# Kernel optimization log

Hardware: AMD Instinct MI355X
Metric: run time of the kernel (lower is better)

Reference implementation:

```python
import jax, jax.numpy as jnp
import numpy as np

T, N, E = 8, 10000, 200000
F_IN, H, OUT = 32, 128, 64
EPS = 1e-5


def setup_inputs() -> dict:
    key = jax.random.key(0)
    ks = jax.random.split(key, 28)
    inp = {}
    inp['x'] = jax.random.normal(ks[0], (T, N, F_IN), jnp.float32)
    inp['edge_index'] = jax.random.randint(ks[1], (2, E), 0, N, dtype=jnp.int32)
    # GCN layer weights (Glorot-ish scale)
    inp['w_gcn0'] = jax.random.normal(ks[2], (F_IN, H), jnp.float32) / np.float32(np.sqrt(F_IN))
    inp['b_gcn0'] = jnp.zeros((H,), jnp.float32)
    inp['w_gcn1'] = jax.random.normal(ks[3], (H, H), jnp.float32) / np.float32(np.sqrt(H))
    inp['b_gcn1'] = jnp.zeros((H,), jnp.float32)
    inp['w_gcn2'] = jax.random.normal(ks[4], (H, H), jnp.float32) / np.float32(np.sqrt(H))
    inp['b_gcn2'] = jnp.zeros((H,), jnp.float32)
    # BatchNorm (eval mode) params for the two inner norms
    for i, kb in zip(range(2), range(5, 9, 2)):
        inp[f'bn_g{i}'] = 1.0 + 0.1 * jax.random.normal(ks[kb], (H,), jnp.float32)
        inp[f'bn_b{i}'] = 0.1 * jax.random.normal(ks[kb + 1], (H,), jnp.float32)
        inp[f'bn_m{i}'] = 0.1 * jax.random.normal(ks[kb + 10], (H,), jnp.float32)
        inp[f'bn_v{i}'] = jax.random.uniform(ks[kb + 11], (H,), jnp.float32, 0.5, 1.5)
    # 3-layer LSTM params, torch gate order (i, f, g, o)
    s = np.float32(1.0 / np.sqrt(OUT))
    dims_in = [H, OUT, OUT]
    for l in range(3):
        k0, k1, k2, k3 = jax.random.split(ks[20 + l], 4)
        inp[f'w_ih_{l}'] = jax.random.uniform(k0, (4 * OUT, dims_in[l]), jnp.float32, -s, s)
        inp[f'w_hh_{l}'] = jax.random.uniform(k1, (4 * OUT, OUT), jnp.float32, -s, s)
        inp[f'b_ih_{l}'] = jax.random.uniform(k2, (4 * OUT,), jnp.float32, -s, s)
        inp[f'b_hh_{l}'] = jax.random.uniform(k3, (4 * OUT,), jnp.float32, -s, s)
    return inp


def reference(x, edge_index, w_gcn0, b_gcn0, w_gcn1, b_gcn1, w_gcn2, b_gcn2,
              bn_g0, bn_b0, bn_m0, bn_v0, bn_g1, bn_b1, bn_m1, bn_v1,
              w_ih_0, w_hh_0, b_ih_0, b_hh_0,
              w_ih_1, w_hh_1, b_ih_1, b_hh_1,
              w_ih_2, w_hh_2, b_ih_2, b_hh_2):
    src, dst = edge_index[0], edge_index[1]
    # symmetric GCN normalization with self-loops: deg = in-degree + 1
    deg = jax.ops.segment_sum(jnp.ones((E,), x.dtype), dst, num_segments=N) + 1.0
    dis = jax.lax.rsqrt(deg)
    coef = dis[src] * dis[dst]          # [E] edge norm
    self_w = dis * dis                   # [N] self-loop norm

    def gcn(h, W, b):
        hw = jnp.einsum('tnf,fo->tno', h, W)                      # [T,N,O]
        msg = hw[:, src, :] * coef[None, :, None]                  # [T,E,O]
        agg = jax.vmap(lambda m: jax.ops.segment_sum(m, dst, num_segments=N))(msg)
        return agg + hw * self_w[None, :, None] + b

    def bn(h, g, b_, m, v):  # eval-mode BatchNorm1d
        return (h - m) * (g * jax.lax.rsqrt(v + EPS)) + b_

    h = bn(jax.nn.relu(gcn(x, w_gcn0, b_gcn0)), bn_g0, bn_b0, bn_m0, bn_v0)
    h = bn(jax.nn.relu(gcn(h, w_gcn1, b_gcn1)), bn_g1, bn_b1, bn_m1, bn_v1)
    h = jax.nn.relu(gcn(h, w_gcn2, b_gcn2))                        # [T,N,H]

    def lstm_layer(xs, Wih, Whh, bih, bhh):
        Hd = Whh.shape[1]
        bias = bih + bhh
        def step(carry, xt):
            hp, cp = carry
            g = xt @ Wih.T + hp @ Whh.T + bias
            i, f, gg, o = jnp.split(g, 4, axis=-1)
            c = jax.nn.sigmoid(f) * cp + jax.nn.sigmoid(i) * jnp.tanh(gg)
            hn = jax.nn.sigmoid(o) * jnp.tanh(c)
            return (hn, c), hn
        z = jnp.zeros((xs.shape[1], Hd), xs.dtype)
        _, ys = jax.lax.scan(step, (z, z), xs)
        return ys  # [T,N,Hd]

    ys = lstm_layer(h, w_ih_0, w_hh_0, b_ih_0, b_hh_0)
    ys = lstm_layer(ys, w_ih_1, w_hh_1, b_ih_1, b_hh_1)
    ys = lstm_layer(ys, w_ih_2, w_hh_2, b_ih_2, b_hh_2)
    return ys[-1]  # [N, OUT] == x[:, -1, :] in the torch code
```

## Files before the change

### kernel.cpp

```cpp
#include <hip/hip_runtime.h>
#include <hip/hip_bf16.h>
#include <math.h>

#define NTHREADS 256
#define T_STEPS 8
#define F_INC 32
#define H_DIM 128
#define O_DIM 64

typedef unsigned short u16;
typedef __attribute__((ext_vector_type(8))) short short8_t;
typedef __attribute__((ext_vector_type(4))) float float4_t;

__device__ __forceinline__ float bf2f(u16 u) {
    return __uint_as_float(((unsigned)u) << 16);
}
__device__ __forceinline__ u16 f2bf(float f) {
    __hip_bfloat16 h = __float2bfloat16(f);
    union { __hip_bfloat16 h; u16 s; } cv; cv.h = h; return cv.s;
}
__device__ __forceinline__ void bf8_unpack(uint4 u, float* f) {
    f[0] = __uint_as_float(u.x << 16); f[1] = __uint_as_float(u.x & 0xffff0000u);
    f[2] = __uint_as_float(u.y << 16); f[3] = __uint_as_float(u.y & 0xffff0000u);
    f[4] = __uint_as_float(u.z << 16); f[5] = __uint_as_float(u.z & 0xffff0000u);
    f[6] = __uint_as_float(u.w << 16); f[7] = __uint_as_float(u.w & 0xffff0000u);
}
__device__ __forceinline__ float fsig(float x) {
    float xc = fminf(fmaxf(x, -30.f), 30.f);
    float e = __builtin_amdgcn_exp2f(xc * -1.4426950408889634f);
    return __builtin_amdgcn_rcpf(1.0f + e);
}
__device__ __forceinline__ float ftanh(float x) {
    float xc = fminf(fmaxf(x, -15.f), 15.f);
    float e = __builtin_amdgcn_exp2f(xc * -2.8853900817779268f);
    float r = __builtin_amdgcn_rcpf(1.0f + e);
    return fmaf(-2.0f * e, r, 1.0f);
}

__global__ void count_kernel(const int* __restrict__ ei, int* __restrict__ cnt, int E) {
    int e = blockIdx.x * NTHREADS + threadIdx.x;
    if (e < E) atomicAdd(&cnt[ei[E + e]], 1);
}

__global__ void scan_part1(const int* __restrict__ cnt, int* __restrict__ bsum, int n) {
    __shared__ int sd[NTHREADS];
    const int i = blockIdx.x * NTHREADS + threadIdx.x;
    sd[threadIdx.x] = (i < n) ? cnt[i] : 0;
    __syncthreads();
    for (int off = 128; off > 0; off >>= 1) {
        if (threadIdx.x < off) sd[threadIdx.x] += sd[threadIdx.x + off];
        __syncthreads();
    }
    if (threadIdx.x == 0) bsum[blockIdx.x] = sd[0];
}

__global__ void scan_part3(const int* __restrict__ cnt, const int* __restrict__ bsum,
                           int* __restrict__ rowptr, int* __restrict__ wp,
                           float* __restrict__ dis, float* __restrict__ selfw, int n) {
    __shared__ int sd[NTHREADS];
    __shared__ int sbase;
    const int tid = threadIdx.x;
    if (tid < 64) {
        int v0 = (tid < blockIdx.x) ? bsum[tid] : 0;
        #pragma unroll
        for (int off = 1; off < 64; off <<= 1) v0 += __shfl_xor(v0, off);
        if (tid == 0) sbase = v0;
    }
    const int i = blockIdx.x * NTHREADS + tid;
    const int v = (i < n) ? cnt[i] : 0;
    sd[tid] = v;
    __syncthreads();
    for (int off = 1; off < NTHREADS; off <<= 1) {
        const int tv = (tid >= off) ? sd[tid - off] : 0;
        __syncthreads();
        sd[tid] += tv;
        __syncthreads();
    }
    const int excl = sbase + sd[tid] - v;
    if (i < n) {
        rowptr[i] = excl; wp[i] = excl;
        if (i == n - 1) rowptr[n] = excl + v;
        const float d = 1.0f + (float)v;
        dis[i] = rsqrtf(d);
        selfw[i] = 1.0f / d;
    }
}

__global__ void fill_kernel(const int* __restrict__ ei, const float* __restrict__ dis,
                            int* __restrict__ wp, int* __restrict__ csr_src,
                            float* __restrict__ coefA, int E) {
    int e = blockIdx.x * NTHREADS + threadIdx.x;
    if (e < E) {
        int s = ei[e], d = ei[E + e];
        int p = atomicAdd(&wp[d], 1);
        csr_src[p] = s;
        coefA[p] = dis[s] * dis[d];
    }
}

__global__ void wprep_all_kernel(const float* g0, const float* g1, const float* g2,
                                 const float* i0, const float* i1, const float* i2,
                                 const float* h0, const float* h1, const float* h2,
                                 u16* o_g0, u16* o_g1, u16* o_g2,
                                 u16* o_i0, u16* o_i1, u16* o_i2,
                                 u16* o_h0, u16* o_h1, u16* o_h2) {
    const int i = blockIdx.x * NTHREADS + threadIdx.x;
    if (i < 4096)        { o_g0[i] = f2bf(g0[(i & 31) * 128 + (i >> 5)]); }
    else if (i < 20480)  { int j = i - 4096;   o_g1[j] = f2bf(g1[(j & 127) * 128 + (j >> 7)]); }
    else if (i < 36864)  { int j = i - 20480;  o_g2[j] = f2bf(g2[(j & 127) * 128 + (j >> 7)]); }
    else if (i < 69632)  { int j = i - 36864;  o_i0[j] = f2bf(i0[j]); }
    else if (i < 86016)  { int j = i - 69632;  o_i1[j] = f2bf(i1[j]); }
    else if (i < 102400) { int j = i - 86016;  o_i2[j] = f2bf(i2[j]); }
    else if (i < 118784) { int j = i - 102400; o_h0[j] = f2bf(h0[j]); }
    else if (i < 135168) { int j = i - 118784; o_h1[j] = f2bf(h1[j]); }
    else if (i < 151552) { int j = i - 135168; o_h2[j] = f2bf(h2[j]); }
}

__global__ __launch_bounds__(NTHREADS)
void gcn32_kernel(const float* __restrict__ x, const int* __restrict__ rowptr,
                  const int* __restrict__ csrc, const float* __restrict__ coefA,
                  const float* __restrict__ selfw, const u16* __restrict__ Wt,
                  const float* __restrict__ bias,
                  const float* __restrict__ bng, const float* __restrict__ bnb,
                  const float* __restrict__ bnm, const float* __restrict__ bnv,
                  u16* __restrict__ out, int N) {
    constexpr int ASTR = 40;
    __shared__ __align__(16) u16 aT[16][ASTR];
    const int t = blockIdx.x;
    const int n0 = blockIdx.y * 16;
    const int tid = threadIdx.x;
    const int wid = tid >> 6, lane = tid & 63;
    const int quad = lane >> 4, l16 = lane & 15;
    const float* xb = x + (long)t * N * 32;

    const int split = lane >> 3;
    const int c4 = (lane & 7) * 4;
    for (int i = 0; i < 4; ++i) {
        const int n = n0 + wid * 4 + i;
        const int e0 = rowptr[n], e1 = rowptr[n + 1];
        float a[4] = {};
        #pragma unroll 2
        for (int e = e0 + split; e < e1; e += 8) {
            const float wgt = coefA[e];
            const int s = csrc[e];
            const float4 v = *(const float4*)(xb + (long)s * 32 + c4);
            a[0] = fmaf(wgt, v.x, a[0]);
            a[1] = fmaf(wgt, v.y, a[1]);
            a[2] = fmaf(wgt, v.z, a[2]);
            a[3] = fmaf(wgt, v.w, a[3]);
        }
        #pragma unroll
        for (int j = 0; j < 4; ++j) {
            a[j] += __shfl_xor(a[j], 8);
            a[j] += __shfl_xor(a[j], 16);
            a[j] += __shfl_xor(a[j], 32);
        }
        if (split == 0) {
            const float sw = selfw[n];
            const float4 sv = *(const float4*)(xb + (long)n * 32 + c4);
            ushort4 o;
            o.x = f2bf(fmaf(sw, sv.x, a[0]));
            o.y = f2bf(fmaf(sw, sv.y, a[1]));
            o.z = f2bf(fmaf(sw, sv.z, a[2]));
            o.w = f2bf(fmaf(sw, sv.w, a[3]));
            *(ushort4*)(&aT[wid * 4 + i][c4]) = o;
        }
    }
    __syncthreads();

    const short8_t fA = *(const short8_t*)(&aT[l16][quad * 8]);
    float4_t acc[2];
    short8_t fB[2];
    #pragma unroll
    for (int ct = 0; ct < 2; ++ct) {
        const int col = wid * 32 + ct * 16 + l16;
        fB[ct] = *(const short8_t*)(Wt + (long)col * 32 + quad * 8);
        acc[ct] = (float4_t){0.f, 0.f, 0.f, 0.f};
    }
    #pragma unroll
    for (int ct = 0; ct < 2; ++ct)
        acc[ct] = __builtin_amdgcn_mfma_f32_16x16x32_bf16(fA, fB[ct], acc[ct], 0, 0, 0);

    #pragma unroll
    for (int ct = 0; ct < 2; ++ct) {
        const int c = wid * 32 + ct * 16 + l16;
        const float s = bng[c] * rsqrtf(bnv[c] + 1e-5f);
        const float a1 = bnb[c] - bnm[c] * s;
        const float a0 = bias[c];
        #pragma unroll
        for (int r = 0; r < 4; ++r) {
            const int node = quad * 4 + r;
            float v = fmaf(fmaxf(acc[ct][r] + a0, 0.f), s, a1);
            out[((long)t * N + n0 + node) * 128 + c] = f2bf(v);
        }
    }
}

template<int EPI>
__global__ __launch_bounds__(NTHREADS)
void gcn128_kernel(const u16* __restrict__ h, const int* __restrict__ rowptr,
                   const int* __restrict__ csrc, const float* __restrict__ coefA,
                   const float* __restrict__ selfw, const u16* __restrict__ Wt,
                   const float* __restrict__ bias,
                   const float* __restrict__ bng, const float* __restrict__ bnb,
                   const float* __restrict__ bnm, const float* __restrict__ bnv,
                   u16* __restrict__ out, int N) {
    constexpr int ASTR = 136;
    __shared__ __align__(16) u16 aT[16][ASTR];
    const int t = blockIdx.x;
    const int n0 = blockIdx.y * 16;
    const int tid = threadIdx.x;
    const int wid = tid >> 6, lane = tid & 63;
    const int quad = lane >> 4, l16 = lane & 15;
    const u16* hb = h + (long)t * N * 128;

    const int split = lane >> 4;
    const int c8 = l16 * 8;
    for (int i = 0; i < 4; ++i) {
        const int n = n0 + wid * 4 + i;
        const int e0 = rowptr[n], e1 = rowptr[n + 1];
        float a[8] = {};
        #pragma unroll 2
        for (int e = e0 + split; e < e1; e += 4) {
            const float wgt = coefA[e];
            const int s = csrc[e];
            const uint4 v = *(const uint4*)(hb + (long)s * 128 + c8);
            float f[8];
            bf8_unpack(v, f);
            #pragma unroll
            for (int j = 0; j < 8; ++j) a[j] = fmaf(wgt, f[j], a[j]);
        }
        #pragma unroll
        for (int j = 0; j < 8; ++j) {
            a[j] += __shfl_xor(a[j], 16);
            a[j] += __shfl_xor(a[j], 32);
        }
        if (split == 0) {
            const float sw = selfw[n];
            const uint4 sv = *(const uint4*)(hb + (long)n * 128 + c8);
            float f[8];
            bf8_unpack(sv, f);
            ushort4 o0, o1;
            o0.x = f2bf(fmaf(sw, f[0], a[0])); o0.y = f2bf(fmaf(sw, f[1], a[1]));
            o0.z = f2bf(fmaf(sw, f[2], a[2])); o0.w = f2bf(fmaf(sw, f[3], a[3]));
            o1.x = f2bf(fmaf(sw, f[4], a[4])); o1.y = f2bf(fmaf(sw, f[5], a[5]));
            o1.z = f2bf(fmaf(sw, f[6], a[6])); o1.w = f2bf(fmaf(sw, f[7], a[7]));
            *(ushort4*)(&aT[wid * 4 + i][c8]) = o0;
            *(ushort4*)(&aT[wid * 4 + i][c8 + 4]) = o1;
        }
    }
    __syncthreads();

    short8_t fA[4];
    #pragma unroll
    for (int ks = 0; ks < 4; ++ks)
        fA[ks] = *(const short8_t*)(&aT[l16][ks * 32 + quad * 8]);
    float4_t acc[2];
    #pragma unroll
    for (int ct = 0; ct < 2; ++ct) acc[ct] = (float4_t){0.f, 0.f, 0.f, 0.f};
    #pragma unroll
    for (int ct = 0; ct < 2; ++ct) {
        const int col = wid * 32 + ct * 16 + l16;
        #pragma unroll
        for (int ks = 0; ks < 4; ++ks) {
            const short8_t fB = *(const short8_t*)(Wt + (long)col * 128 + ks * 32 + quad * 8);
            acc[ct] = __builtin_amdgcn_mfma_f32_16x16x32_bf16(fA[ks], fB, acc[ct], 0, 0, 0);
        }
    }

    #pragma unroll
    for (int ct = 0; ct < 2; ++ct) {
        const int c = wid * 32 + ct * 16 + l16;
        const float a0 = bias[c];
        float s = 0.f, a1 = 0.f;
        if constexpr (EPI == 2) {
            s = bng[c] * rsqrtf(bnv[c] + 1e-5f);
            a1 = bnb[c] - bnm[c] * s;
        }
        #pragma unroll
        for (int r = 0; r < 4; ++r) {
            const int node = quad * 4 + r;
            float v = fmaxf(acc[ct][r] + a0, 0.f);
            if constexpr (EPI == 2) v = fmaf(v, s, a1);
            out[((long)t * N + n0 + node) * 128 + c] = f2bf(v);
        }
    }
}

template<int KIN, bool IN_SPLIT, bool LAST>
__global__ __launch_bounds__(NTHREADS, 2)
void lstm_layer_kernel(const u16* __restrict__ in_hi, const u16* __restrict__ in_lo,
                       const u16* __restrict__ wih, const u16* __restrict__ whh,
                       const float* __restrict__ bi, const float* __restrict__ bh,
                       u16* __restrict__ out_hi, u16* __restrict__ out_lo,
                       float* __restrict__ out_f, int N) {
    constexpr int NKS = KIN / 32;
    constexpr int HSTR = 76;
    const int tid = threadIdx.x;
    const int w = tid >> 6, lane = tid & 63;
    const int quad = lane >> 4, l16 = lane & 15;
    const int n0 = blockIdx.x * 16;
    const int u = w * 16 + l16;

    __shared__ __align__(16) u16 hT[2][16][HSTR];
    for (int p = tid; p < 2 * 16 * HSTR; p += NTHREADS) (&hT[0][0][0])[p] = 0;

    short8_t fI[4][NKS], fH[4][2];
    #pragma unroll
    for (int g = 0; g < 4; ++g) {
        #pragma unroll
        for (int ks = 0; ks < NKS; ++ks)
            fI[g][ks] = *(const short8_t*)(wih + (long)(g * 64 + u) * KIN + ks * 32 + quad * 8);
        #pragma unroll
        for (int ks = 0; ks < 2; ++ks)
            fH[g][ks] = *(const short8_t*)(whh + (long)(g * 64 + u) * 64 + ks * 32 + quad * 8);
    }
    float bias[4];
    #pragma unroll
    for (int g = 0; g < 4; ++g) bias[g] = bi[g * 64 + u] + bh[g * 64 + u];
    float cst[4] = {};
    __syncthreads();

    #pragma unroll 1
    for (int t = 0; t < T_STEPS; ++t) {
        short8_t ain[NKS], ainl[NKS];
        const long ibase = ((long)t * N + n0 + l16) * KIN + quad * 8;
        #pragma unroll
        for (int ks = 0; ks < NKS; ++ks) {
            ain[ks] = *(const short8_t*)(in_hi + ibase + ks * 32);
            if constexpr (IN_SPLIT) ainl[ks] = *(const short8_t*)(in_lo + ibase + ks * 32);
        }
        short8_t ah[2], al[2];
        #pragma unroll
        for (int ks = 0; ks < 2; ++ks) {
            ah[ks] = *(const short8_t*)(&hT[0][l16][ks * 32 + quad * 8]);
            al[ks] = *(const short8_t*)(&hT[1][l16][ks * 32 + quad * 8]);
        }
        __syncthreads();

        float4_t acc[4];
        #pragma unroll
        for (int g = 0; g < 4; ++g) acc[g] = (float4_t){bias[g], bias[g], bias[g], bias[g]};
        #pragma unroll
        for (int ks = 0; ks < NKS; ++ks)
            #pragma unroll
            for (int g = 0; g < 4; ++g) {
                acc[g] = __builtin_amdgcn_mfma_f32_16x16x32_bf16(ain[ks], fI[g][ks], acc[g], 0, 0, 0);
                if constexpr (IN_SPLIT)
                    acc[g] = __builtin_amdgcn_mfma_f32_16x16x32_bf16(ainl[ks], fI[g][ks], acc[g], 0, 0, 0);
            }
        #pragma unroll
        for (int ks = 0; ks < 2; ++ks)
            #pragma unroll
            for (int g = 0; g < 4; ++g) {
                acc[g] = __builtin_amdgcn_mfma_f32_16x16x32_bf16(ah[ks], fH[g][ks], acc[g], 0, 0, 0);
                acc[g] = __builtin_amdgcn_mfma_f32_16x16x32_bf16(al[ks], fH[g][ks], acc[g], 0, 0, 0);
            }

        #pragma unroll
        for (int r = 0; r < 4; ++r) {
            const float si = fsig(acc[0][r]);
            const float sf = fsig(acc[1][r]);
            const float gg = ftanh(acc[2][r]);
            const float so = fsig(acc[3][r]);
            const float c = sf * cst[r] + si * gg;
            cst[r] = c;
            const float h = so * ftanh(c);
            const int node = quad * 4 + r;
            const u16 hi = f2bf(h);
            const u16 lo = f2bf(h - bf2f(hi));
            hT[0][node][u] = hi;
            hT[1][node][u] = lo;
            if constexpr (LAST) {
                if (t == T_STEPS - 1) out_f[(long)(n0 + node) * 64 + u] = h;
            } else {
                const long o = ((long)t * N + n0 + node) * 64 + u;
                out_hi[o] = hi;
                out_lo[o] = lo;
            }
        }
        __syncthreads();
    }
}

extern "C" void kernel_launch(void* const* d_in, const int* in_sizes, int n_in,
                              void* d_out, int out_size, void* d_ws, size_t ws_size,
                              hipStream_t stream) {
    (void)n_in; (void)out_size; (void)ws_size;
    const float* x      = (const float*)d_in[0];
    const int*   ei     = (const int*)d_in[1];
    const float* w_gcn0 = (const float*)d_in[2];
    const float* b_gcn0 = (const float*)d_in[3];
    const float* w_gcn1 = (const float*)d_in[4];
    const float* b_gcn1 = (const float*)d_in[5];
    const float* w_gcn2 = (const float*)d_in[6];
    const float* b_gcn2 = (const float*)d_in[7];
    const float* bn_g0  = (const float*)d_in[8];
    const float* bn_b0  = (const float*)d_in[9];
    const float* bn_m0  = (const float*)d_in[10];
    const float* bn_v0  = (const float*)d_in[11];
    const float* bn_g1  = (const float*)d_in[12];
    const float* bn_b1  = (const float*)d_in[13];
    const float* bn_m1  = (const float*)d_in[14];
    const float* bn_v1  = (const float*)d_in[15];
    const float* w_ih_0 = (const float*)d_in[16];
    const float* w_hh_0 = (const float*)d_in[17];
    const float* b_ih_0 = (const float*)d_in[18];
    const float* b_hh_0 = (const float*)d_in[19];
    const float* w_ih_1 = (const float*)d_in[20];
    const float* w_hh_1 = (const float*)d_in[21];
    const float* b_ih_1 = (const float*)d_in[22];
    const float* b_hh_1 = (const float*)d_in[23];
    const float* w_ih_2 = (const float*)d_in[24];
    const float* w_hh_2 = (const float*)d_in[25];
    const float* b_ih_2 = (const float*)d_in[26];
    const float* b_hh_2 = (const float*)d_in[27];

    const int E = in_sizes[1] / 2;
    const int N = in_sizes[0] / (T_STEPS * F_INC);
    const long M = (long)N * T_STEPS;

    char* ws = (char*)d_ws;
    size_t off = 0;
    auto carve = [&](size_t bytes) -> void* {
        void* p = ws + off;
        off += (bytes + 255) & ~(size_t)255;
        return p;
    };
    float* dis     = (float*)carve((size_t)N * 4);
    float* selfw   = (float*)carve((size_t)N * 4);
    float* coefA   = (float*)carve((size_t)E * 4);
    int*   cnt     = (int*)carve((size_t)N * 4);
    int*   rowptr  = (int*)carve((size_t)(N + 1) * 4);
    int*   wp      = (int*)carve((size_t)N * 4);
    int*   csr_src = (int*)carve((size_t)E * 4);
    int*   bsum    = (int*)carve(64 * 4);
    u16*   hbuf    = (u16*)carve((size_t)M * H_DIM * 2);
    u16*   hbuf2   = (u16*)carve((size_t)M * H_DIM * 2);
    u16*   pA_hi   = (u16*)carve((size_t)M * O_DIM * 2);
    u16*   pA_lo   = (u16*)carve((size_t)M * O_DIM * 2);
    u16*   pB_hi   = (u16*)carve((size_t)M * O_DIM * 2);
    u16*   pB_lo   = (u16*)carve((size_t)M * O_DIM * 2);
    u16*   wt0     = (u16*)carve((size_t)128 * 32 * 2);
    u16*   wt1     = (u16*)carve((size_t)128 * 128 * 2);
    u16*   wt2     = (u16*)carve((size_t)128 * 128 * 2);
    u16*   wtih0   = (u16*)carve((size_t)256 * 128 * 2);
    u16*   wtih1   = (u16*)carve((size_t)256 * 64 * 2);
    u16*   wtih2   = (u16*)carve((size_t)256 * 64 * 2);
    u16*   whh0b   = (u16*)carve((size_t)256 * 64 * 2);
    u16*   whh1b   = (u16*)carve((size_t)256 * 64 * 2);
    u16*   whh2b   = (u16*)carve((size_t)256 * 64 * 2);

    const dim3 b256(NTHREADS);
    const int gN = (N + NTHREADS - 1) / NTHREADS;
    const int gE = (E + NTHREADS - 1) / NTHREADS;

    hipMemsetAsync(cnt, 0, (size_t)N * 4, stream);
    count_kernel<<<gE, b256, 0, stream>>>(ei, cnt, E);
    scan_part1<<<gN, b256, 0, stream>>>(cnt, bsum, N);
    scan_part3<<<gN, b256, 0, stream>>>(cnt, bsum, rowptr, wp, dis, selfw, N);
    fill_kernel<<<gE, b256, 0, stream>>>(ei, dis, wp, csr_src, coefA, E);

    wprep_all_kernel<<<(151552 + 255) / 256, b256, 0, stream>>>(
        w_gcn0, w_gcn1, w_gcn2, w_ih_0, w_ih_1, w_ih_2, w_hh_0, w_hh_1, w_hh_2,
        wt0, wt1, wt2, wtih0, wtih1, wtih2, whh0b, whh1b, whh2b);

    const dim3 gG(T_STEPS, N / 16);
    gcn32_kernel<<<gG, b256, 0, stream>>>(
        x, rowptr, csr_src, coefA, selfw, wt0, b_gcn0,
        bn_g0, bn_b0, bn_m0, bn_v0, hbuf, N);
    gcn128_kernel<2><<<gG, b256, 0, stream>>>(
        hbuf, rowptr, csr_src, coefA, selfw, wt1, b_gcn1,
        bn_g1, bn_b1, bn_m1, bn_v1, hbuf2, N);
    gcn128_kernel<1><<<gG, b256, 0, stream>>>(
        hbuf2, rowptr, csr_src, coefA, selfw, wt2, b_gcn2,
        nullptr, nullptr, nullptr, nullptr, hbuf, N);

    const int gL = N / 16;
    lstm_layer_kernel<128, false, false><<<gL, b256, 0, stream>>>(
        hbuf, nullptr, wtih0, whh0b, b_ih_0, b_hh_0, pA_hi, pA_lo, nullptr, N);
    lstm_layer_kernel<64, true, false><<<gL, b256, 0, stream>>>(
        pA_hi, pA_lo, wtih1, whh1b, b_ih_1, b_hh_1, pB_hi, pB_lo, nullptr, N);
    lstm_layer_kernel<64, true, true><<<gL, b256, 0, stream>>>(
        pB_hi, pB_lo, wtih2, whh2b, b_ih_2, b_hh_2, nullptr, nullptr, (float*)d_out, N);
}
```

Baseline: 370.4 us.

## Pack CSR edge src/coef into int2 and stage block edges in LDS

Combines the CSR source index and normalization coefficient into a single int2 array so one 8-byte load replaces two scattered 4-byte loads. Each GCN block cooperatively copies the edge metadata for its 16 destination nodes into shared memory before aggregating, with a global-memory fallback for edges beyond a 1024-entry cap. The aggregation loop now reads metadata from LDS and unrolls deeper. This adds a __syncthreads and 8KB of LDS per block, which may reduce occupancy.

Measured after the change: 361.0 us. 1.03x faster.

```diff
diff --git a/kernel.cpp b/kernel.cpp
--- a/kernel.cpp
+++ b/kernel.cpp
@@ -87,14 +87,12 @@
 }
 
 __global__ void fill_kernel(const int* __restrict__ ei, const float* __restrict__ dis,
-                            int* __restrict__ wp, int* __restrict__ csr_src,
-                            float* __restrict__ coefA, int E) {
+                            int* __restrict__ wp, int2* __restrict__ epk, int E) {
     int e = blockIdx.x * NTHREADS + threadIdx.x;
     if (e < E) {
         int s = ei[e], d = ei[E + e];
         int p = atomicAdd(&wp[d], 1);
-        csr_src[p] = s;
-        coefA[p] = dis[s] * dis[d];
+        epk[p] = make_int2(s, __float_as_int(dis[s] * dis[d]));
     }
 }
 
@@ -118,14 +116,16 @@
 
 __global__ __launch_bounds__(NTHREADS)
 void gcn32_kernel(const float* __restrict__ x, const int* __restrict__ rowptr,
-                  const int* __restrict__ csrc, const float* __restrict__ coefA,
+                  const int2* __restrict__ epk,
                   const float* __restrict__ selfw, const u16* __restrict__ Wt,
                   const float* __restrict__ bias,
                   const float* __restrict__ bng, const float* __restrict__ bnb,
                   const float* __restrict__ bnm, const float* __restrict__ bnv,
                   u16* __restrict__ out, int N) {
     constexpr int ASTR = 40;
+    constexpr int ECAP = 1024;
     __shared__ __align__(16) u16 aT[16][ASTR];
+    __shared__ int2 sM[ECAP];
     const int t = blockIdx.x;
     const int n0 = blockIdx.y * 16;
     const int tid = threadIdx.x;
@@ -133,17 +133,35 @@
     const int quad = lane >> 4, l16 = lane & 15;
     const float* xb = x + (long)t * N * 32;
 
+    const int eb0 = rowptr[n0];
+    const int ecnt = min(rowptr[n0 + 16] - eb0, ECAP);
+    for (int p = tid; p < ecnt; p += NTHREADS) sM[p] = epk[eb0 + p];
+    __syncthreads();
+
     const int split = lane >> 3;
     const int c4 = (lane & 7) * 4;
     for (int i = 0; i < 4; ++i) {
         const int n = n0 + wid * 4 + i;
-        const int e0 = rowptr[n], e1 = rowptr[n + 1];
+        const int l0 = rowptr[n] - eb0;
+        const int l1 = rowptr[n + 1] - eb0;
+        const int eL = min(l1, ecnt);
+        const int start = l0 + split;
         float a[4] = {};
-        #pragma unroll 2
-        for (int e = e0 + split; e < e1; e += 8) {
-            const float wgt = coefA[e];
-            const int s = csrc[e];
-            const float4 v = *(const float4*)(xb + (long)s * 32 + c4);
+        #pragma unroll 4
+        for (int e = start; e < eL; e += 8) {
+            const int2 m = sM[e];
+            const float wgt = __int_as_float(m.y);
+            const float4 v = *(const float4*)(xb + (long)m.x * 32 + c4);
+            a[0] = fmaf(wgt, v.x, a[0]);
+            a[1] = fmaf(wgt, v.y, a[1]);
+            a[2] = fmaf(wgt, v.z, a[2]);
+            a[3] = fmaf(wgt, v.w, a[3]);
+        }
+        const int kL = (eL > start) ? (eL - start + 7) >> 3 : 0;
+        for (int e = start + kL * 8; e < l1; e += 8) {
+            const int2 m = epk[eb0 + e];
+            const float wgt = __int_as_float(m.y);
+            const float4 v = *(const float4*)(xb + (long)m.x * 32 + c4);
             a[0] = fmaf(wgt, v.x, a[0]);
             a[1] = fmaf(wgt, v.y, a[1]);
             a[2] = fmaf(wgt, v.z, a[2]);
@@ -199,14 +217,16 @@
 template<int EPI>
 __global__ __launch_bounds__(NTHREADS)
 void gcn128_kernel(const u16* __restrict__ h, const int* __restrict__ rowptr,
-                   const int* __restrict__ csrc, const float* __restrict__ coefA,
+                   const int2* __restrict__ epk,
                    const float* __restrict__ selfw, const u16* __restrict__ Wt,
                    const float* __restrict__ bias,
                    const float* __restrict__ bng, const float* __restrict__ bnb,
                    const float* __restrict__ bnm, const float* __restrict__ bnv,
                    u16* __restrict__ out, int N) {
     constexpr int ASTR = 136;
+    constexpr int ECAP = 1024;
     __shared__ __align__(16) u16 aT[16][ASTR];
+    __shared__ int2 sM[ECAP];
     const int t = blockIdx.x;
     const int n0 = blockIdx.y * 16;
     const int tid = threadIdx.x;
@@ -214,17 +234,35 @@
     const int quad = lane >> 4, l16 = lane & 15;
     const u16* hb = h + (long)t * N * 128;
 
+    const int eb0 = rowptr[n0];
+    const int ecnt = min(rowptr[n0 + 16] - eb0, ECAP);
+    for (int p = tid; p < ecnt; p += NTHREADS) sM[p] = epk[eb0 + p];
+    __syncthreads();
+
     const int split = lane >> 4;
     const int c8 = l16 * 8;
     for (int i = 0; i < 4; ++i) {
         const int n = n0 + wid * 4 + i;
-        const int e0 = rowptr[n], e1 = rowptr[n + 1];
+        const int l0 = rowptr[n] - eb0;
+        const int l1 = rowptr[n + 1] - eb0;
+        const int eL = min(l1, ecnt);
+        const int start = l0 + split;
         float a[8] = {};
-        #pragma unroll 2
-        for (int e = e0 + split; e < e1; e += 4) {
-            const float wgt = coefA[e];
-            const int s = csrc[e];
-            const uint4 v = *(const uint4*)(hb + (long)s * 128 + c8);
+        #pragma unroll 4
+        for (int e = start; e < eL; e += 4) {
+            const int2 m = sM[e];
+            const float wgt = __int_as_float(m.y);
+            const uint4 v = *(const uint4*)(hb + (long)m.x * 128 + c8);
+            float f[8];
+            bf8_unpack(v, f);
+            #pragma unroll
+            for (int j = 0; j < 8; ++j) a[j] = fmaf(wgt, f[j], a[j]);
+        }
+        const int kL = (eL > start) ? (eL - start + 3) >> 2 : 0;
+        for (int e = start + kL * 4; e < l1; e += 4) {
+            const int2 m = epk[eb0 + e];
+            const float wgt = __int_as_float(m.y);
+            const uint4 v = *(const uint4*)(hb + (long)m.x * 128 + c8);
             float f[8];
             bf8_unpack(v, f);
             #pragma unroll
@@ -429,11 +467,10 @@
     };
     float* dis     = (float*)carve((size_t)N * 4);
     float* selfw   = (float*)carve((size_t)N * 4);
-    float* coefA   = (float*)carve((size_t)E * 4);
     int*   cnt     = (int*)carve((size_t)N * 4);
     int*   rowptr  = (int*)carve((size_t)(N + 1) * 4);
     int*   wp      = (int*)carve((size_t)N * 4);
-    int*   csr_src = (int*)carve((size_t)E * 4);
+    int2*  epk     = (int2*)carve((size_t)E * 8);
     int*   bsum    = (int*)carve(64 * 4);
     u16*   hbuf    = (u16*)carve((size_t)M * H_DIM * 2);
     u16*   hbuf2   = (u16*)carve((size_t)M * H_DIM * 2);
@@ -459,7 +496,7 @@
     count_kernel<<<gE, b256, 0, stream>>>(ei, cnt, E);
     scan_part1<<<gN, b256, 0, stream>>>(cnt, bsum, N);
     scan_part3<<<gN, b256, 0, stream>>>(cnt, bsum, rowptr, wp, dis, selfw, N);
-    fill_kernel<<<gE, b256, 0, stream>>>(ei, dis, wp, csr_src, coefA, E);
+    fill_kernel<<<gE, b256, 0, stream>>>(ei, dis, wp, epk, E);
 
     wprep_all_kernel<<<(151552 + 255) / 256, b256, 0, stream>>>(
         w_gcn0, w_gcn1, w_gcn2, w_ih_0, w_ih_1, w_ih_2, w_hh_0, w_hh_1, w_hh_2,
@@ -467,13 +504,13 @@
 
     const dim3 gG(T_STEPS, N / 16);
     gcn32_kernel<<<gG, b256, 0, stream>>>(
-        x, rowptr, csr_src, coefA, selfw, wt0, b_gcn0,
+        x, rowptr, epk, selfw, wt0, b_gcn0,
         bn_g0, bn_b0, bn_m0, bn_v0, hbuf, N);
     gcn128_kernel<2><<<gG, b256, 0, stream>>>(
-        hbuf, rowptr, csr_src, coefA, selfw, wt1, b_gcn1,
+        hbuf, rowptr, epk, selfw, wt1, b_gcn1,
         bn_g1, bn_b1, bn_m1, bn_v1, hbuf2, N);
     gcn128_kernel<1><<<gG, b256, 0, stream>>>(
-        hbuf2, rowptr, csr_src, coefA, selfw, wt2, b_gcn2,
+        hbuf2, rowptr, epk, selfw, wt2, b_gcn2,
         nullptr, nullptr, nullptr, nullptr, hbuf, N);
 
     const int gL = N / 16;
```
